# Performance work log

Hardware: AMD Instinct MI355X
Metric: run time of the kernel (lower is better)

## Reference

```python
import jax, jax.numpy as jnp
import numpy as np

B, CIN, COUT, H, W = 4, 64, 64, 128, 160
K = 3          # kernel size
KK = K * K     # 9 sample positions
EPS = 1e-8     # torch cosine_similarity eps


def setup_inputs() -> dict:
    key = jax.random.key(0)
    k1, k2, k3, k4 = jax.random.split(key, 4)
    x = jax.random.normal(k1, (B, CIN, H, W), jnp.float32)
    stdv = 1.0 / np.sqrt(CIN * K * K)
    weight = jax.random.uniform(k2, (COUT, CIN, K, K), jnp.float32, -stdv, stdv)
    bias = jnp.zeros((COUT,), jnp.float32)
    cm_in = CIN + KK - 1          # x concat with 8 similarity maps
    cm_out = 3 * KK               # o1 | o2 | mask
    # module zero-inits these; use small random values so offsets are nontrivial
    cm_weight = jax.random.normal(k3, (cm_out, cm_in, K, K), jnp.float32) * 0.01
    cm_bias = jax.random.normal(k4, (cm_out,), jnp.float32) * 0.01
    return {"x": x, "weight": weight, "bias": bias,
            "cm_weight": cm_weight, "cm_bias": cm_bias}


def _conv3x3(x, w, b):
    y = jax.lax.conv_general_dilated(x, w, (1, 1), ((1, 1), (1, 1)),
                                     dimension_numbers=("NCHW", "OIHW", "NCHW"))
    return y + b[None, :, None, None]


def _unfold3x3(x):
    # F.unfold(x, 3, padding=1) -> [B, C, 9, H, W]
    Hx, Wx = x.shape[2], x.shape[3]
    xp = jnp.pad(x, ((0, 0), (0, 0), (1, 1), (1, 1)))
    return jnp.stack([xp[:, :, i:i + Hx, j:j + Wx]
                      for i in range(K) for j in range(K)], axis=2)


def _similarity(x):
    p = _unfold3x3(x)                       # [B,C,9,H,W]
    c = p[:, :, KK // 2:KK // 2 + 1]        # center patch [B,C,1,H,W]
    dot = jnp.sum(c * p, axis=1)            # [B,9,H,W]
    nc = jnp.sqrt(jnp.sum(c * c, axis=1))
    nk = jnp.sqrt(jnp.sum(p * p, axis=1))
    cos = dot / (jnp.maximum(nc, EPS) * jnp.maximum(nk, EPS))
    # drop center (always 1): [B,8,H,W]
    return jnp.concatenate([cos[:, :KK // 2], cos[:, KK // 2 + 1:]], axis=1)


def _deform_conv(x, offset, mask, weight, bias):
    Bx, C, Hx, Wx = x.shape
    # DCNv2 layout: per sample position k, channel 2k = dy, 2k+1 = dx
    off = offset.reshape(Bx, KK, 2, Hx, Wx)
    dy, dx = off[:, :, 0], off[:, :, 1]                    # [B,9,H,W]
    ky = jnp.repeat(jnp.arange(K), K) - 1                  # kernel row offsets
    kx = jnp.tile(jnp.arange(K), K) - 1                    # kernel col offsets
    py = dy + jnp.arange(Hx)[None, None, :, None] + ky[None, :, None, None]
    px = dx + jnp.arange(Wx)[None, None, None, :] + kx[None, :, None, None]
    y0 = jnp.floor(py)
    x0 = jnp.floor(px)
    wy1 = (py - y0)[:, None]    # [B,1,9,H,W]
    wx1 = (px - x0)[:, None]
    y0i = y0.astype(jnp.int32)
    x0i = x0.astype(jnp.int32)
    x_flat = x.reshape(Bx, C, Hx * Wx)

    def gather(yi, xi):
        valid = (yi >= 0) & (yi < Hx) & (xi >= 0) & (xi < Wx)
        idx = jnp.clip(yi, 0, Hx - 1) * Wx + jnp.clip(xi, 0, Wx - 1)
        idxf = jnp.broadcast_to(idx.reshape(Bx, 1, -1), (Bx, C, KK * Hx * Wx))
        v = jnp.take_along_axis(x_flat, idxf, axis=2).reshape(Bx, C, KK, Hx, Wx)
        return v * valid[:, None].astype(v.dtype)

    g00 = gather(y0i, x0i)
    g01 = gather(y0i, x0i + 1)
    g10 = gather(y0i + 1, x0i)
    g11 = gather(y0i + 1, x0i + 1)
    val = (g00 * (1 - wy1) * (1 - wx1) + g01 * (1 - wy1) * wx1
           + g10 * wy1 * (1 - wx1) + g11 * wy1 * wx1)      # [B,C,9,H,W]
    val = val * mask[:, None]                              # modulated
    out = jnp.einsum("bckhw,ock->bohw", val,
                     weight.reshape(weight.shape[0], C, KK))
    return out + bias[None, :, None, None]


def reference(x, weight, bias, cm_weight, cm_bias):
    sim = _similarity(x)
    om = _conv3x3(jnp.concatenate([x, sim], axis=1), cm_weight, cm_bias)
    o1, o2, m = jnp.split(om, 3, axis=1)
    offset = jnp.concatenate([o1, o2], axis=1)
    mask = jax.nn.sigmoid(m)
    return _deform_conv(x, offset, mask, weight, bias)
```

## Files before the change

kernel.cpp:

```cpp
#include <hip/hip_runtime.h>
#include <math.h>

#define B_    4
#define CIN_  64
#define COUT_ 64
#define H_    128
#define W_    160
#define HW_   (H_*W_)
#define NPIX_ (B_*HW_)
#define XC_   72
#define EPS_  1e-8f
#define NCH_  21

typedef float     f4    __attribute__((ext_vector_type(4)));
typedef float     f32x4 __attribute__((ext_vector_type(4)));
typedef _Float16  h8    __attribute__((ext_vector_type(8)));
typedef _Float16  h4    __attribute__((ext_vector_type(4)));

__global__ __launch_bounds__(256) void prep_kernel(const float* __restrict__ wt,
                                                   const float* __restrict__ cmw,
                                                   _Float16* __restrict__ wlin,
                                                   _Float16* __restrict__ cwL)
{
    int i = blockIdx.x * 256 + threadIdx.x;
    if (i < 9*4096) {
        int k = i >> 12, r = i & 4095;
        int j = r >> 10, s = (r >> 9) & 1, lane = (r >> 3) & 63, e = i & 7;
        int o = j*16 + (lane & 15);
        int c = s*32 + ((lane >> 4) << 3) + e;
        wlin[i] = (_Float16)wt[(o*64 + c)*9 + k];
    }
    int jj = i - 9*4096;
    if (jj >= 0 && jj < NCH_*1024) {
        int CH = jj >> 10, s = (jj >> 9) & 1, lane = (jj >> 3) & 63, e = jj & 7;
        int o  = s*16 + (lane & 15);
        int kk = ((lane >> 4) << 3) + e;
        int k  = CH*32 + kk;
        _Float16 v = (_Float16)0.f;
        if (o < 27 && k < 648) {
            int tap = k / 72, ch = k - (k/72)*72;
            v = (_Float16)cmw[((size_t)o*72 + ch)*9 + tap];
        }
        cwL[jj] = v;
    }
}

__global__ __launch_bounds__(128) void xpose_kernel(const float* __restrict__ x,
                                                    _Float16* __restrict__ xsh)
{
    __shared__ float l[128][65];
    const int t = threadIdx.x;
    const int px0 = blockIdx.x * 128;
    const int b = px0 / HW_, p0 = px0 % HW_;
    for (int c = 0; c < 64; c++)
        l[t][c] = x[((size_t)(b*64 + c))*HW_ + p0 + t];
    __syncthreads();
#pragma unroll
    for (int rep = 0; rep < 16; rep++) {
        int pxl = (t >> 4) + rep*8;
        int c4  = (t & 15) * 4;
        h4 v = { (_Float16)l[pxl][c4],   (_Float16)l[pxl][c4+1],
                 (_Float16)l[pxl][c4+2], (_Float16)l[pxl][c4+3] };
        *reinterpret_cast<h4*>(&xsh[(size_t)(px0+pxl)*XC_ + c4]) = v;
    }
}

__global__ __launch_bounds__(64, 5) void sim_kernel(_Float16* __restrict__ xsh)
{
    const int t = threadIdx.x;
    const int wg = blockIdx.x;
    const int sw = (wg & 7) * 640 + (wg >> 3);
    const int px = sw * 16 + (t >> 2);
    const int q = t & 3;
    const int w = px % W_, hh = (px / W_) % H_, b = px / HW_;

    const _Float16* cen = xsh + (size_t)px * XC_ + q*16;
    float cv[16]; float ncc = 0.f;
#pragma unroll
    for (int s = 0; s < 2; s++) {
        h8 cb = *reinterpret_cast<const h8*>(cen + s*8);
#pragma unroll
        for (int j = 0; j < 8; j++) {
            float v = (float)cb[j];
            cv[s*8+j] = v;
            ncc = fmaf(v, v, ncc);
        }
    }

    const int kyA[8] = {-1,-1,-1, 0, 0, 1, 1, 1};
    const int kxA[8] = {-1, 0, 1,-1, 1,-1, 0, 1};
    float dot[8], nn[8];
#pragma unroll
    for (int n = 0; n < 8; n++) {
        int hn = hh + kyA[n], wn = w + kxA[n];
        bool v = (hn >= 0) & (hn < H_) & (wn >= 0) & (wn < W_);
        float msk = v ? 1.f : 0.f;
        const _Float16* nb = xsh + (size_t)(b*HW_ + min(max(hn,0),H_-1)*W_ + min(max(wn,0),W_-1))*XC_ + q*16;
        float d = 0.f, s2 = 0.f;
#pragma unroll
        for (int s = 0; s < 2; s++) {
            h8 qb = *reinterpret_cast<const h8*>(nb + s*8);
#pragma unroll
            for (int j = 0; j < 8; j++) {
                float vv = (float)qb[j] * msk;
                d  = fmaf(cv[s*8+j], vv, d);
                s2 = fmaf(vv, vv, s2);
            }
        }
        dot[n] = d; nn[n] = s2;
    }
    ncc += __shfl_xor(ncc, 1); ncc += __shfl_xor(ncc, 2);
    const float ncr = 1.f / fmaxf(sqrtf(ncc), EPS_);
    float res[8];
#pragma unroll
    for (int n = 0; n < 8; n++) {
        float dt = dot[n]; dt += __shfl_xor(dt, 1); dt += __shfl_xor(dt, 2);
        float s2 = nn[n];  s2 += __shfl_xor(s2, 1); s2 += __shfl_xor(s2, 2);
        res[n] = dt * ncr / fmaxf(sqrtf(s2), EPS_);
    }
    if (q < 2) {
        h4 r = { (_Float16)res[q*4],   (_Float16)res[q*4+1],
                 (_Float16)res[q*4+2], (_Float16)res[q*4+3] };
        *reinterpret_cast<h4*>(xsh + (size_t)px * XC_ + 64 + q*4) = r;
    }
}

__global__ __launch_bounds__(256, 3) void cmdcn_kernel(const _Float16* __restrict__ xsh,
                                                       const _Float16* __restrict__ cwL,
                                                       const float* __restrict__ cmb,
                                                       const _Float16* __restrict__ wlin,
                                                       const float* __restrict__ bias,
                                                       float* __restrict__ out)
{
    __shared__ float om_l[64][29];

    const int t  = threadIdx.x;
    const int wg = blockIdx.x;
    const int sw = (wg & 7) * 160 + (wg >> 3);
    const int px0 = sw * 64;
    const int lane = t & 63, wv = t >> 6;
    const int fr = lane & 15, fq = lane >> 4;

    const int pxs = px0 + wv*16 + fr;
    const int wsx = pxs % W_, hs = (pxs / W_) % H_, bs = pxs / HW_;
    const size_t xrow = (size_t)bs * HW_;

    {
        f32x4 acc[2];
        acc[0] = (f32x4){0.f,0.f,0.f,0.f};
        acc[1] = (f32x4){0.f,0.f,0.f,0.f};

        h8 G8; h8 WF[2]; bool mskb;

#define CM_ISSUE_G(CH) do {                                                   \
    int k0_ = (CH)*32 + fq*8;                                                 \
    int tap_ = (k0_ * 911) >> 16;                                             \
    bool valid_ = (tap_ < 9);                                                 \
    tap_ = min(tap_, 8);                                                      \
    int ch_ = min(max(k0_ - tap_*72, 0), 64);                                 \
    int t3_ = (tap_ * 11) >> 5;                                               \
    int hy_ = hs + t3_ - 1, wx_ = wsx + (tap_ - t3_*3) - 1;                   \
    bool v_ = (hy_ >= 0) & (hy_ < H_) & (wx_ >= 0) & (wx_ < W_);              \
    mskb = v_ & valid_;                                                       \
    const _Float16* src_ = xsh + (size_t)(xrow + min(max(hy_,0),H_-1)*W_      \
                                          + min(max(wx_,0),W_-1))*XC_ + ch_;  \
    G8 = *reinterpret_cast<const h8*>(src_);                                  \
  } while(0)

#define CM_ISSUE_W(CH) do {                                                   \
    const _Float16* wp_ = cwL + (CH)*1024 + lane*8;                           \
    WF[0] = *reinterpret_cast<const h8*>(wp_);                                \
    WF[1] = *reinterpret_cast<const h8*>(wp_ + 512);                          \
  } while(0)

        CM_ISSUE_G(0);
        CM_ISSUE_W(0);

#pragma unroll 1
        for (int c = 0; c < NCH_; c++) {
            h8 zero8 = {(_Float16)0.f,(_Float16)0.f,(_Float16)0.f,(_Float16)0.f,
                        (_Float16)0.f,(_Float16)0.f,(_Float16)0.f,(_Float16)0.f};
            h8 AF = mskb ? G8 : zero8;
            h8 W0 = WF[0], W1 = WF[1];
            if (c < NCH_-1) { CM_ISSUE_G(c+1); CM_ISSUE_W(c+1); }
            acc[0] = __builtin_amdgcn_mfma_f32_16x16x32_f16(AF, W0, acc[0], 0,0,0);
            acc[1] = __builtin_amdgcn_mfma_f32_16x16x32_f16(AF, W1, acc[1], 0,0,0);
        }

        const int rl = wv*16 + fq*4;
#pragma unroll
        for (int j = 0; j < 2; j++) {
            int o = j*16 + fr;
            if (o < 27) {
                float bv = cmb[o];
#pragma unroll
                for (int r = 0; r < 4; r++)
                    om_l[rl + r][o] = acc[j][r] + bv;
            }
        }
    }
    __syncthreads();

    const int ce = fq * 8;
    const int rp = wv*16 + fr;
    const int lb = lane*8;

    f32x4 acc[4];
#pragma unroll
    for (int j = 0; j < 4; j++) acc[j] = (f32x4){0.f,0.f,0.f,0.f};

#define DCN_META(KK, W00, W01, W10, W11, P0, P1, P2, P3) do {                 \
    float dy_ = om_l[rp][2*(KK)], dx_ = om_l[rp][2*(KK)+1];                   \
    float mz_ = om_l[rp][18+(KK)];                                            \
    float m_  = 1.f / (1.f + __expf(-mz_));                                   \
    float py_ = (float)(hs + (KK)/3 - 1) + dy_;                               \
    float px_ = (float)(wsx + (KK)%3 - 1) + dx_;                              \
    float y0f_ = floorf(py_), x0f_ = floorf(px_);                             \
    int   y0_ = (int)y0f_,   x0_ = (int)x0f_;                                 \
    float wy_ = py_ - y0f_,  wx_ = px_ - x0f_;                                \
    bool vy0_ = (y0_ >= 0)  & (y0_ < H_);                                     \
    bool vy1_ = (y0_ >= -1) & (y0_ < H_ - 1);                                 \
    bool vx0_ = (x0_ >= 0)  & (x0_ < W_);                                     \
    bool vx1_ = (x0_ >= -1) & (x0_ < W_ - 1);                                 \
    W00 = (1.f-wy_)*(1.f-wx_)*m_*((vy0_&vx0_)?1.f:0.f);                       \
    W01 = (1.f-wy_)*wx_      *m_*((vy0_&vx1_)?1.f:0.f);                       \
    W10 = wy_*(1.f-wx_)      *m_*((vy1_&vx0_)?1.f:0.f);                       \
    W11 = wy_*wx_            *m_*((vy1_&vx1_)?1.f:0.f);                       \
    int y0c_ = min(max(y0_,   0), H_-1), y1c_ = min(max(y0_+1, 0), H_-1);     \
    int x0c_ = min(max(x0_,   0), W_-1), x1c_ = min(max(x0_+1, 0), W_-1);     \
    P0 = xsh + (size_t)(xrow + y0c_*W_ + x0c_)*XC_ + ce;                      \
    P1 = xsh + (size_t)(xrow + y0c_*W_ + x1c_)*XC_ + ce;                      \
    P2 = xsh + (size_t)(xrow + y1c_*W_ + x0c_)*XC_ + ce;                      \
    P3 = xsh + (size_t)(xrow + y1c_*W_ + x1c_)*XC_ + ce;                      \
  } while(0)

#define DCN_GATHER(G, P0, P1, P2, P3) do {                                    \
    G[0] = *reinterpret_cast<const h8*>(P0);                                  \
    G[1] = *reinterpret_cast<const h8*>(P0 + 32);                             \
    G[2] = *reinterpret_cast<const h8*>(P1);                                  \
    G[3] = *reinterpret_cast<const h8*>(P1 + 32);                             \
    G[4] = *reinterpret_cast<const h8*>(P2);                                  \
    G[5] = *reinterpret_cast<const h8*>(P2 + 32);                             \
    G[6] = *reinterpret_cast<const h8*>(P3);                                  \
    G[7] = *reinterpret_cast<const h8*>(P3 + 32);                             \
  } while(0)

#define DCN_WLOAD(KK, WF) do {                                                \
    const _Float16* wp_ = wlin + (KK)*4096 + lb;                              \
    WF[0] = *reinterpret_cast<const h8*>(wp_);                                \
    WF[1] = *reinterpret_cast<const h8*>(wp_ + 512);                          \
    WF[2] = *reinterpret_cast<const h8*>(wp_ + 1024);                         \
    WF[3] = *reinterpret_cast<const h8*>(wp_ + 1536);                         \
    WF[4] = *reinterpret_cast<const h8*>(wp_ + 2048);                         \
    WF[5] = *reinterpret_cast<const h8*>(wp_ + 2560);                         \
    WF[6] = *reinterpret_cast<const h8*>(wp_ + 3072);                         \
    WF[7] = *reinterpret_cast<const h8*>(wp_ + 3584);                         \
  } while(0)

#define DCN_COMBINE(G, W00, W01, W10, W11, AA, AB) do {                       \
    _Float16 h00 = (_Float16)(W00), h01 = (_Float16)(W01);                    \
    _Float16 h10 = (_Float16)(W10), h11 = (_Float16)(W11);                    \
    h8 v00 = {h00,h00,h00,h00,h00,h00,h00,h00};                               \
    h8 v01 = {h01,h01,h01,h01,h01,h01,h01,h01};                               \
    h8 v10 = {h10,h10,h10,h10,h10,h10,h10,h10};                               \
    h8 v11 = {h11,h11,h11,h11,h11,h11,h11,h11};                               \
    AA = v00*G[0] + v01*G[2] + v10*G[4] + v11*G[6];                           \
    AB = v00*G[1] + v01*G[3] + v10*G[5] + v11*G[7];                           \
  } while(0)

#define DCN_MFMA(WF, AA, AB) do {                                             \
    acc[0] = __builtin_amdgcn_mfma_f32_16x16x32_f16(AA, WF[0], acc[0],0,0,0); \
    acc[0] = __builtin_amdgcn_mfma_f32_16x16x32_f16(AB, WF[1], acc[0],0,0,0); \
    acc[1] = __builtin_amdgcn_mfma_f32_16x16x32_f16(AA, WF[2], acc[1],0,0,0); \
    acc[1] = __builtin_amdgcn_mfma_f32_16x16x32_f16(AB, WF[3], acc[1],0,0,0); \
    acc[2] = __builtin_amdgcn_mfma_f32_16x16x32_f16(AA, WF[4], acc[2],0,0,0); \
    acc[2] = __builtin_amdgcn_mfma_f32_16x16x32_f16(AB, WF[5], acc[2],0,0,0); \
    acc[3] = __builtin_amdgcn_mfma_f32_16x16x32_f16(AA, WF[6], acc[3],0,0,0); \
    acc[3] = __builtin_amdgcn_mfma_f32_16x16x32_f16(AB, WF[7], acc[3],0,0,0); \
  } while(0)

    float wA00, wA01, wA10, wA11; const _Float16 *pA0, *pA1, *pA2, *pA3;
    float wB00, wB01, wB10, wB11; const _Float16 *pB0, *pB1, *pB2, *pB3;
    h8 GA[8], GB[8];

    DCN_META(0, wA00,wA01,wA10,wA11, pA0,pA1,pA2,pA3);
    DCN_GATHER(GA, pA0,pA1,pA2,pA3);
    DCN_META(1, wB00,wB01,wB10,wB11, pB0,pB1,pB2,pB3);

#pragma unroll 1
    for (int kp = 0; kp < 4; kp++) {
        const int ke = kp*2;
        DCN_GATHER(GB, pB0,pB1,pB2,pB3);
        h8 WE[8]; DCN_WLOAD(ke, WE);
        float nA00,nA01,nA10,nA11; const _Float16 *qA0,*qA1,*qA2,*qA3;
        DCN_META(ke+2, nA00,nA01,nA10,nA11, qA0,qA1,qA2,qA3);
        h8 aA, aB; DCN_COMBINE(GA, wA00,wA01,wA10,wA11, aA, aB);
        DCN_MFMA(WE, aA, aB);
        wA00=nA00; wA01=nA01; wA10=nA10; wA11=nA11;
        pA0=qA0; pA1=qA1; pA2=qA2; pA3=qA3;
        DCN_GATHER(GA, pA0,pA1,pA2,pA3);

        h8 WO[8]; DCN_WLOAD(ke+1, WO);
        float nB00,nB01,nB10,nB11; const _Float16 *qB0,*qB1,*qB2,*qB3;
        if (kp < 3) {
            DCN_META(ke+3, nB00,nB01,nB10,nB11, qB0,qB1,qB2,qB3);
        } else {
            nB00=wB00; nB01=wB01; nB10=wB10; nB11=wB11;
            qB0=pB0; qB1=pB1; qB2=pB2; qB3=pB3;
        }
        h8 cA, cB; DCN_COMBINE(GB, wB00,wB01,wB10,wB11, cA, cB);
        DCN_MFMA(WO, cA, cB);
        wB00=nB00; wB01=nB01; wB10=nB10; wB11=nB11;
        pB0=qB0; pB1=qB1; pB2=qB2; pB3=qB3;
    }

    {
        h8 WE[8]; DCN_WLOAD(8, WE);
        h8 aA, aB; DCN_COMBINE(GA, wA00,wA01,wA10,wA11, aA, aB);
        DCN_MFMA(WE, aA, aB);
    }

    const int bo = px0 / HW_, po = px0 % HW_;
#pragma unroll
    for (int j = 0; j < 4; j++) {
        int o = j*16 + fr;
        float bv = bias[o];
        f4 r = { acc[j][0] + bv, acc[j][1] + bv, acc[j][2] + bv, acc[j][3] + bv };
        *reinterpret_cast<f4*>(&out[((size_t)(bo*64 + o))*HW_ + po + wv*16 + fq*4]) = r;
    }
}

extern "C" void kernel_launch(void* const* d_in, const int* in_sizes, int n_in,
                              void* d_out, int out_size, void* d_ws, size_t ws_size,
                              hipStream_t stream)
{
    const float* x   = (const float*)d_in[0];
    const float* wt  = (const float*)d_in[1];
    const float* bs  = (const float*)d_in[2];
    const float* cmw = (const float*)d_in[3];
    const float* cmb = (const float*)d_in[4];
    float* out = (float*)d_out;

    _Float16* xsh  = (_Float16*)d_ws;
    _Float16* wlin = xsh + (size_t)NPIX_ * XC_;
    _Float16* cwL  = wlin + 9*4096;

    prep_kernel <<<228, 256, 0, stream>>>(wt, cmw, wlin, cwL);
    xpose_kernel<<<NPIX_/128, 128, 0, stream>>>(x, xsh);
    sim_kernel  <<<NPIX_/16,  64,  0, stream>>>(xsh);
    cmdcn_kernel<<<NPIX_/64,  256, 0, stream>>>(xsh, cwL, cmb, wlin, bs, out);
}
```

Before: 79.44 us.

## Fuse transpose and similarity kernels via LDS halo tile; double-buffer cm loads

Merges the fp32→fp16 NHWC transpose and the cosine-similarity pass into one kernel. Each 320-thread block loads a 3-row by 82-column halo tile of all 64 channels into LDS, computes the 8 neighbour similarities from LDS, and writes both the transposed features and the similarity maps. This removes one launch and the sim kernel's global re-reads of the neighbours. The cost is redundant halo loads (three input rows per output row) and strided, non-coalesced-friendly channel reads in the load loop. Separately, the offset-conv MFMA loop is unrolled by two with two register sets, so loads are issued two chunks ahead, at the price of more registers.

```diff
diff --git a/kernel.cpp b/kernel.cpp
--- a/kernel.cpp
+++ b/kernel.cpp
@@ -45,36 +45,33 @@
     }
 }
 
-__global__ __launch_bounds__(128) void xpose_kernel(const float* __restrict__ x,
-                                                    _Float16* __restrict__ xsh)
+__global__ __launch_bounds__(320) void xpose_sim_kernel(const float* __restrict__ x,
+                                                        _Float16* __restrict__ xsh)
 {
-    __shared__ float l[128][65];
-    const int t = threadIdx.x;
-    const int px0 = blockIdx.x * 128;
-    const int b = px0 / HW_, p0 = px0 % HW_;
-    for (int c = 0; c < 64; c++)
-        l[t][c] = x[((size_t)(b*64 + c))*HW_ + p0 + t];
+    __shared__ _Float16 lds[3][82][72];
+
+    const int t  = threadIdx.x;
+    const int wg = blockIdx.x;
+    const int sw = (wg & 7) * 128 + (wg >> 3);
+    const int px0 = sw * 80;
+    const int b  = px0 / HW_;
+    const int h  = (px0 % HW_) / W_;
+    const int w0 = px0 % W_;
+
+    for (int i = t; i < 192*82; i += 320) {
+        int task = i / 82;
+        int e    = i - task*82;
+        int r3   = task >> 6, c = task & 63;
+        int hy   = min(max(h + r3 - 1, 0), H_-1);
+        int wxc  = min(max(w0 - 1 + e, 0), W_-1);
+        lds[r3][e][c] = (_Float16)x[(size_t)(b*64 + c)*HW_ + hy*W_ + wxc];
+    }
     __syncthreads();
-#pragma unroll
-    for (int rep = 0; rep < 16; rep++) {
-        int pxl = (t >> 4) + rep*8;
-        int c4  = (t & 15) * 4;
-        h4 v = { (_Float16)l[pxl][c4],   (_Float16)l[pxl][c4+1],
-                 (_Float16)l[pxl][c4+2], (_Float16)l[pxl][c4+3] };
-        *reinterpret_cast<h4*>(&xsh[(size_t)(px0+pxl)*XC_ + c4]) = v;
-    }
-}
-
-__global__ __launch_bounds__(64, 5) void sim_kernel(_Float16* __restrict__ xsh)
-{
-    const int t = threadIdx.x;
-    const int wg = blockIdx.x;
-    const int sw = (wg & 7) * 640 + (wg >> 3);
-    const int px = sw * 16 + (t >> 2);
-    const int q = t & 3;
-    const int w = px % W_, hh = (px / W_) % H_, b = px / HW_;
-
-    const _Float16* cen = xsh + (size_t)px * XC_ + q*16;
+
+    const int pxl = t >> 2, q = t & 3;
+    const int w = w0 + pxl;
+    const _Float16* cen = &lds[1][1 + pxl][q*16];
+
     float cv[16]; float ncc = 0.f;
 #pragma unroll
     for (int s = 0; s < 2; s++) {
@@ -92,10 +89,10 @@
     float dot[8], nn[8];
 #pragma unroll
     for (int n = 0; n < 8; n++) {
-        int hn = hh + kyA[n], wn = w + kxA[n];
+        int hn = h + kyA[n], wn = w + kxA[n];
         bool v = (hn >= 0) & (hn < H_) & (wn >= 0) & (wn < W_);
         float msk = v ? 1.f : 0.f;
-        const _Float16* nb = xsh + (size_t)(b*HW_ + min(max(hn,0),H_-1)*W_ + min(max(wn,0),W_-1))*XC_ + q*16;
+        const _Float16* nb = &lds[1 + kyA[n]][1 + pxl + kxA[n]][q*16];
         float d = 0.f, s2 = 0.f;
 #pragma unroll
         for (int s = 0; s < 2; s++) {
@@ -118,10 +115,14 @@
         float s2 = nn[n];  s2 += __shfl_xor(s2, 1); s2 += __shfl_xor(s2, 2);
         res[n] = dt * ncr / fmaxf(sqrtf(s2), EPS_);
     }
+
+    _Float16* op = xsh + (size_t)(px0 + pxl) * XC_ + q*16;
+    *reinterpret_cast<h8*>(op)     = *reinterpret_cast<const h8*>(cen);
+    *reinterpret_cast<h8*>(op + 8) = *reinterpret_cast<const h8*>(cen + 8);
     if (q < 2) {
         h4 r = { (_Float16)res[q*4],   (_Float16)res[q*4+1],
                  (_Float16)res[q*4+2], (_Float16)res[q*4+3] };
-        *reinterpret_cast<h4*>(xsh + (size_t)px * XC_ + 64 + q*4) = r;
+        *reinterpret_cast<h4*>(xsh + (size_t)(px0 + pxl) * XC_ + 64 + q*4) = r;
     }
 }
 
@@ -150,9 +151,7 @@
         acc[0] = (f32x4){0.f,0.f,0.f,0.f};
         acc[1] = (f32x4){0.f,0.f,0.f,0.f};
 
-        h8 G8; h8 WF[2]; bool mskb;
-
-#define CM_ISSUE_G(CH) do {                                                   \
+#define CM_ISSUE_G(CH, G8, MSK) do {                                          \
     int k0_ = (CH)*32 + fq*8;                                                 \
     int tap_ = (k0_ * 911) >> 16;                                             \
     bool valid_ = (tap_ < 9);                                                 \
@@ -161,31 +160,53 @@
     int t3_ = (tap_ * 11) >> 5;                                               \
     int hy_ = hs + t3_ - 1, wx_ = wsx + (tap_ - t3_*3) - 1;                   \
     bool v_ = (hy_ >= 0) & (hy_ < H_) & (wx_ >= 0) & (wx_ < W_);              \
-    mskb = v_ & valid_;                                                       \
+    MSK = v_ & valid_;                                                        \
     const _Float16* src_ = xsh + (size_t)(xrow + min(max(hy_,0),H_-1)*W_      \
                                           + min(max(wx_,0),W_-1))*XC_ + ch_;  \
     G8 = *reinterpret_cast<const h8*>(src_);                                  \
   } while(0)
 
-#define CM_ISSUE_W(CH) do {                                                   \
+#define CM_ISSUE_W(CH, WF) do {                                               \
     const _Float16* wp_ = cwL + (CH)*1024 + lane*8;                           \
     WF[0] = *reinterpret_cast<const h8*>(wp_);                                \
     WF[1] = *reinterpret_cast<const h8*>(wp_ + 512);                          \
   } while(0)
 
-        CM_ISSUE_G(0);
-        CM_ISSUE_W(0);
+#define CM_MFMA(G8, MSK, WF) do {                                             \
+    h8 zero8_ = {(_Float16)0.f,(_Float16)0.f,(_Float16)0.f,(_Float16)0.f,     \
+                 (_Float16)0.f,(_Float16)0.f,(_Float16)0.f,(_Float16)0.f};    \
+    h8 AF_ = (MSK) ? (G8) : zero8_;                                           \
+    acc[0] = __builtin_amdgcn_mfma_f32_16x16x32_f16(AF_, WF[0], acc[0],0,0,0);\
+    acc[1] = __builtin_amdgcn_mfma_f32_16x16x32_f16(AF_, WF[1], acc[1],0,0,0);\
+  } while(0)
+
+        h8 GAc, GBc; h8 WFA[2], WFB[2]; bool mskA, mskB;
+        CM_ISSUE_G(0, GAc, mskA); CM_ISSUE_W(0, WFA);
+        CM_ISSUE_G(1, GBc, mskB); CM_ISSUE_W(1, WFB);
 
 #pragma unroll 1
-        for (int c = 0; c < NCH_; c++) {
-            h8 zero8 = {(_Float16)0.f,(_Float16)0.f,(_Float16)0.f,(_Float16)0.f,
-                        (_Float16)0.f,(_Float16)0.f,(_Float16)0.f,(_Float16)0.f};
-            h8 AF = mskb ? G8 : zero8;
-            h8 W0 = WF[0], W1 = WF[1];
-            if (c < NCH_-1) { CM_ISSUE_G(c+1); CM_ISSUE_W(c+1); }
-            acc[0] = __builtin_amdgcn_mfma_f32_16x16x32_f16(AF, W0, acc[0], 0,0,0);
-            acc[1] = __builtin_amdgcn_mfma_f32_16x16x32_f16(AF, W1, acc[1], 0,0,0);
-        }
+        for (int cp = 0; cp < 10; cp++) {
+            const int cce = cp*2;
+            {
+                h8 G = GAc; bool m = mskA; h8 W0 = WFA[0], W1 = WFA[1];
+                if (cce + 2 < NCH_) { CM_ISSUE_G(cce+2, GAc, mskA); CM_ISSUE_W(cce+2, WFA); }
+                h8 zero8_ = {(_Float16)0.f,(_Float16)0.f,(_Float16)0.f,(_Float16)0.f,
+                             (_Float16)0.f,(_Float16)0.f,(_Float16)0.f,(_Float16)0.f};
+                h8 AF_ = m ? G : zero8_;
+                acc[0] = __builtin_amdgcn_mfma_f32_16x16x32_f16(AF_, W0, acc[0],0,0,0);
+                acc[1] = __builtin_amdgcn_mfma_f32_16x16x32_f16(AF_, W1, acc[1],0,0,0);
+            }
+            {
+                h8 G = GBc; bool m = mskB; h8 W0 = WFB[0], W1 = WFB[1];
+                if (cce + 3 < NCH_) { CM_ISSUE_G(cce+3, GBc, mskB); CM_ISSUE_W(cce+3, WFB); }
+                h8 zero8_ = {(_Float16)0.f,(_Float16)0.f,(_Float16)0.f,(_Float16)0.f,
+                             (_Float16)0.f,(_Float16)0.f,(_Float16)0.f,(_Float16)0.f};
+                h8 AF_ = m ? G : zero8_;
+                acc[0] = __builtin_amdgcn_mfma_f32_16x16x32_f16(AF_, W0, acc[0],0,0,0);
+                acc[1] = __builtin_amdgcn_mfma_f32_16x16x32_f16(AF_, W1, acc[1],0,0,0);
+            }
+        }
+        CM_MFMA(GAc, mskA, WFA);
 
         const int rl = wv*16 + fq*4;
 #pragma unroll
@@ -345,8 +366,7 @@
     _Float16* wlin = xsh + (size_t)NPIX_ * XC_;
     _Float16* cwL  = wlin + 9*4096;
 
-    prep_kernel <<<228, 256, 0, stream>>>(wt, cmw, wlin, cwL);
-    xpose_kernel<<<NPIX_/128, 128, 0, stream>>>(x, xsh);
-    sim_kernel  <<<NPIX_/16,  64,  0, stream>>>(xsh);
-    cmdcn_kernel<<<NPIX_/64,  256, 0, stream>>>(xsh, cwL, cmb, wlin, bs, out);
+    prep_kernel     <<<228, 256, 0, stream>>>(wt, cmw, wlin, cwL);
+    xpose_sim_kernel<<<NPIX_/80, 320, 0, stream>>>(x, xsh);
+    cmdcn_kernel    <<<NPIX_/64, 256, 0, stream>>>(xsh, cwL, cmb, wlin, bs, out);
 }
```

After: 95.24 us. +19.9%, slower.
